# Kernel tuning notes

Measured on AMD Instinct MI355X. Metric: run time of the kernel, lower is better.

Reference implementation:

```python
import jax, jax.numpy as jnp
import numpy as np

T, B, V, E, H = 128, 32, 32000, 512, 1024
PAD = 0

def setup_inputs() -> dict:
    key = jax.random.key(0)
    ks = jax.random.split(key, 10)
    indices = jax.random.randint(ks[0], (T, B), 0, V)
    emb = jax.random.normal(ks[1], (V, E), jnp.float32) * 0.02
    s = 1.0 / np.sqrt(H).astype(np.float32)
    W_ih = jax.random.normal(ks[2], (4 * H, E), jnp.float32) * s
    W_hh = jax.random.normal(ks[3], (4 * H, H), jnp.float32) * s
    b_ih = jax.random.normal(ks[4], (4 * H,), jnp.float32) * 0.01
    b_hh = jax.random.normal(ks[5], (4 * H,), jnp.float32) * 0.01
    W_out = jax.random.normal(ks[6], (V, H), jnp.float32) * s
    b_out = jnp.zeros((V,), jnp.float32)
    h0 = jax.random.uniform(ks[7], (B, H), jnp.float32, -0.1, 0.1)
    c0 = jax.random.uniform(ks[8], (B, H), jnp.float32, -0.1, 0.1)
    return dict(indices=indices, emb=emb, W_ih=W_ih, W_hh=W_hh,
                b_ih=b_ih, b_hh=b_hh, W_out=W_out, b_out=b_out, h0=h0, c0=c0)

def reference(indices, emb, W_ih, W_hh, b_ih, b_hh, W_out, b_out, h0, c0):
    # embed + relu for all timesteps at once (dropout_rate=0.0 -> identity)
    x_all = jax.nn.relu(emb[indices[:-1]])   # [T-1, B, E]
    targets = indices[1:]                    # [T-1, B]

    def step(carry, inp):
        h, c, loss = carry
        x, tgt = inp
        # torch LSTM gate order: i, f, g, o
        gates = x @ W_ih.T + b_ih + h @ W_hh.T + b_hh   # [B, 4H]
        i, f, g, o = jnp.split(gates, 4, axis=-1)
        c = jax.nn.sigmoid(f) * c + jax.nn.sigmoid(i) * jnp.tanh(g)
        h = jax.nn.sigmoid(o) * jnp.tanh(c)
        logp = jax.nn.log_softmax(h @ W_out.T + b_out, axis=-1)  # [B, V]
        nll = -jnp.take_along_axis(logp, tgt[:, None], axis=-1)[:, 0]
        # NLLLoss(reduction='sum', ignore_index=PAD)
        loss = loss + jnp.sum(jnp.where(tgt != PAD, nll, 0.0))
        return (h, c, loss), None

    (_, _, loss), _ = jax.lax.scan(step, (h0, c0, jnp.float32(0.0)), (x_all, targets))
    return loss
```

## Files before the change

kernel.cpp:

```cpp
#include <hip/hip_runtime.h>
#include <hip/hip_bf16.h>
#include <hip/hip_cooperative_groups.h>
#include <math.h>

namespace cg = cooperative_groups;

typedef __bf16 bf16_t;
typedef bf16_t bf16x8 __attribute__((ext_vector_type(8)));
typedef float f32x4 __attribute__((ext_vector_type(4)));
typedef unsigned u32x2 __attribute__((ext_vector_type(2)));
typedef unsigned u32x4 __attribute__((ext_vector_type(4)));

#define T_SEQ 128
#define NB 32
#define NV 32000
#define NE 512
#define NH 1024
#define G4 4096
#define MROWS 4064
#define MPAD 4096

#define NBLK 256
#define SENT 0xFFFFFFFFu

__device__ __forceinline__ void g2lds16(const bf16_t* g, bf16_t* l) {
  __builtin_amdgcn_global_load_lds((const __attribute__((address_space(1))) void*)g,
                                   (__attribute__((address_space(3))) void*)l, 16, 0, 0);
}

__device__ __forceinline__ unsigned short bf16bits(float x) {
  bf16_t b = (bf16_t)x;
  return __builtin_bit_cast(unsigned short, b);
}

__device__ __forceinline__ void cvt4(const float* __restrict__ s,
                                     bf16_t* __restrict__ d, long j) {
  float4 v = *(const float4*)(s + j * 4);
  uint2 o;
  o.x = (unsigned)bf16bits(v.x) | ((unsigned)bf16bits(v.y) << 16);
  o.y = (unsigned)bf16bits(v.z) | ((unsigned)bf16bits(v.w) << 16);
  *(uint2*)(d + j * 4) = o;
}

__global__ void k_prep(const int* __restrict__ idx, const float* __restrict__ emb,
                       const float* __restrict__ W_ih, const float* __restrict__ W_hh,
                       const float* __restrict__ b_ih, const float* __restrict__ b_hh,
                       const float* __restrict__ W_out, const float* __restrict__ h0,
                       bf16_t* __restrict__ W_ih_bf, bf16_t* __restrict__ W_hh_bf,
                       bf16_t* __restrict__ W_out_bf, bf16_t* __restrict__ x_bf,
                       bf16_t* __restrict__ h_all, bf16_t* __restrict__ h0_bf,
                       float* __restrict__ bc, float* __restrict__ rowS,
                       int* __restrict__ tgt, unsigned* __restrict__ bar) {
  const long n4_Wih = 4096L * 512 / 4;
  const long n4_Whh = 4096L * 1024 / 4;
  const long n4_Wout = 32000L * 1024 / 4;
  const long n4_X = 4096L * 512 / 4;
  const long n4_H0 = 32L * 1024 / 4;
  const long n4_Hall = 4096L * 1024 / 8;
  const long nSentinel = 4064L * 128;
  const long nScal = 3 * 4096L + 1024;
  const long NTOT = n4_Wih + n4_Whh + n4_Wout + n4_X + n4_H0 + n4_Hall + nScal;
  long stride = (long)gridDim.x * blockDim.x;
  for (long i = (long)blockIdx.x * blockDim.x + threadIdx.x; i < NTOT; i += stride) {
    long j = i;
    if (j < n4_Wih) { cvt4(W_ih, W_ih_bf, j); continue; }
    j -= n4_Wih;
    if (j < n4_Whh) { cvt4(W_hh, W_hh_bf, j); continue; }
    j -= n4_Whh;
    if (j < n4_Wout) { cvt4(W_out, W_out_bf, j); continue; }
    j -= n4_Wout;
    if (j < n4_X) {
      long m = j >> 7; int e4 = (int)(j & 127);
      uint2 o; o.x = 0u; o.y = 0u;
      if (m < MROWS) {
        float4 v = *(const float4*)(emb + (long)idx[m] * NE + e4 * 4);
        v.x = fmaxf(v.x, 0.f); v.y = fmaxf(v.y, 0.f);
        v.z = fmaxf(v.z, 0.f); v.w = fmaxf(v.w, 0.f);
        o.x = (unsigned)bf16bits(v.x) | ((unsigned)bf16bits(v.y) << 16);
        o.y = (unsigned)bf16bits(v.z) | ((unsigned)bf16bits(v.w) << 16);
      }
      *(uint2*)(x_bf + m * 512 + e4 * 4) = o;
      continue;
    }
    j -= n4_X;
    if (j < n4_H0) { cvt4(h0, h0_bf, j); continue; }
    j -= n4_H0;
    if (j < n4_Hall) {
      unsigned v = (j < nSentinel) ? SENT : 0u;
      uint4 s; s.x = v; s.y = v; s.z = v; s.w = v;
      ((uint4*)h_all)[j] = s;
      continue;
    }
    j -= n4_Hall;
    if (j < 4096) { bc[j] = b_ih[j] + b_hh[j]; continue; }
    j -= 4096;
    if (j < 4096) { rowS[j] = 0.f; continue; }
    j -= 4096;
    if (j < 4096) { tgt[j] = (j < MROWS) ? idx[j + NB] : 0; continue; }
    j -= 4096;
    { bar[j] = 0u; continue; }
  }
}

__global__ __launch_bounds__(256) void k_gemm1(const bf16_t* __restrict__ A,
                                               const bf16_t* __restrict__ B,
                                               const float* __restrict__ bc,
                                               bf16_t* __restrict__ C) {
  const int K = 512;
  int tid = threadIdx.x, wid = tid >> 6, lane = tid & 63;
  int wm = wid & 1, wn = wid >> 1;
  int quad = lane >> 4, l15 = lane & 15;
  int mBase = blockIdx.x * 64, nBase = blockIdx.y * 128;

  const bf16x8* pa0 = (const bf16x8*)(A + (long)(mBase + wm * 32 + l15) * K + quad * 8);
  const bf16x8* pa1 = (const bf16x8*)(A + (long)(mBase + wm * 32 + 16 + l15) * K + quad * 8);
  const bf16x8* pb[4];
#pragma unroll
  for (int j = 0; j < 4; ++j)
    pb[j] = (const bf16x8*)(B + (long)(nBase + wn * 64 + j * 16 + l15) * K + quad * 8);

  f32x4 acc[2][4];
#pragma unroll
  for (int mi = 0; mi < 2; ++mi)
#pragma unroll
    for (int ni = 0; ni < 4; ++ni) acc[mi][ni] = (f32x4){0.f, 0.f, 0.f, 0.f};

  for (int kk = 0; kk < K / 32; ++kk) {
    bf16x8 a0 = pa0[kk * 4], a1 = pa1[kk * 4];
    bf16x8 b0 = pb[0][kk * 4], b1 = pb[1][kk * 4], b2 = pb[2][kk * 4], b3 = pb[3][kk * 4];
    acc[0][0] = __builtin_amdgcn_mfma_f32_16x16x32_bf16(a0, b0, acc[0][0], 0, 0, 0);
    acc[0][1] = __builtin_amdgcn_mfma_f32_16x16x32_bf16(a0, b1, acc[0][1], 0, 0, 0);
    acc[0][2] = __builtin_amdgcn_mfma_f32_16x16x32_bf16(a0, b2, acc[0][2], 0, 0, 0);
    acc[0][3] = __builtin_amdgcn_mfma_f32_16x16x32_bf16(a0, b3, acc[0][3], 0, 0, 0);
    acc[1][0] = __builtin_amdgcn_mfma_f32_16x16x32_bf16(a1, b0, acc[1][0], 0, 0, 0);
    acc[1][1] = __builtin_amdgcn_mfma_f32_16x16x32_bf16(a1, b1, acc[1][1], 0, 0, 0);
    acc[1][2] = __builtin_amdgcn_mfma_f32_16x16x32_bf16(a1, b2, acc[1][2], 0, 0, 0);
    acc[1][3] = __builtin_amdgcn_mfma_f32_16x16x32_bf16(a1, b3, acc[1][3], 0, 0, 0);
  }
#pragma unroll
  for (int ni = 0; ni < 4; ++ni) {
    int col = nBase + wn * 64 + ni * 16 + l15;
    float bcv = bc[col];
#pragma unroll
    for (int mi = 0; mi < 2; ++mi)
#pragma unroll
      for (int r = 0; r < 4; ++r) {
        int row = mBase + wm * 32 + mi * 16 + quad * 4 + r;
        C[(long)row * G4 + col] = (bf16_t)(acc[mi][ni][r] + bcv);
      }
  }
}

__global__ __launch_bounds__(512) void k_rec9(const bf16_t* __restrict__ gates_x,
                                              const bf16_t* __restrict__ W_hh_bf,
                                              const bf16_t* __restrict__ h0_bf,
                                              bf16_t* __restrict__ h_all,
                                              const float* __restrict__ c0,
                                              unsigned* __restrict__ bar) {
  __shared__ __align__(16) float red[32 * 68];

  int bid = blockIdx.x;
  int mi = bid & 1;
  int hb = bid >> 1;
  int gbase = hb * 8;
  int tid = threadIdx.x, wid = tid >> 6, lane = tid & 63;
  int cg = wid & 1, kh = wid >> 1;
  int quad = lane >> 4, l15 = lane & 15;

  unsigned* genp = bar + mi * 512 + 288;
  unsigned* flagp = bar + mi * 512 + 320 + hb;
  const unsigned* fp2 = bar + mi * 512 + 320 + (lane << 1);
  bool isagg = (bid < 2) && (wid == 7);

  int wrow = (cg ? 2048 : 0) + ((l15 & 8) ? 1024 : 0) + gbase + (l15 & 7);
  const bf16x8* pw = (const bf16x8*)(W_hh_bf + (long)wrow * NH + kh * 256 + quad * 8);
  bf16x8 wfrag[8];
#pragma unroll
  for (int kk = 0; kk < 8; ++kk) wfrag[kk] = pw[kk * 4];

  int pb = tid >> 2, pu2 = (tid & 3) * 2;
  int u0 = gbase + pu2;
  int bglob = mi * 16 + pb;
  float cst0 = 0.f, cst1 = 0.f;
  if (tid < 64) {
    cst0 = c0[(long)bglob * NH + u0];
    cst1 = c0[(long)bglob * NH + u0 + 1];
  }
  unsigned* h32 = (unsigned*)h_all;

  for (int t = 0; t < T_SEQ - 1; ++t) {
    unsigned gxi2 = 0, gxf2 = 0, gxg2 = 0, gxo2 = 0;
    if (tid < 64) {
      const unsigned* gp = (const unsigned*)(gates_x + (long)(t * NB + bglob) * G4);
      int q = u0 >> 1;
      gxi2 = gp[q]; gxf2 = gp[512 + q]; gxg2 = gp[1024 + q]; gxo2 = gp[1536 + q];
    }

    if (t > 0) {
      if (isagg) {
        unsigned need = (unsigned)t;
        while (1) {
          u32x2 fv;
          asm volatile("global_load_dwordx2 %0, %1, off sc0 sc1\n\t"
                       "s_waitcnt vmcnt(0)"
                       : "=&v"(fv) : "v"(fp2) : "memory");
          if (__all((fv.x >= need) & (fv.y >= need))) break;
          __builtin_amdgcn_s_sleep(1);
        }
        if (lane == 0)
          __hip_atomic_store(genp, (unsigned)t, __ATOMIC_RELAXED,
                             __HIP_MEMORY_SCOPE_AGENT);
      }
      if (tid == 0) {
        unsigned need = (unsigned)t;
        while (__hip_atomic_load(genp, __ATOMIC_RELAXED,
                                 __HIP_MEMORY_SCOPE_AGENT) < need)
          __builtin_amdgcn_s_sleep(1);
      }
    }
    __syncthreads();
    asm volatile("" ::: "memory");

    bf16x8 hfr[8];
    if (t == 0) {
      const bf16x8* pa0 =
          (const bf16x8*)(h0_bf + (long)(mi * 16 + l15) * NH + kh * 256 + quad * 8);
#pragma unroll
      for (int kk = 0; kk < 8; ++kk) hfr[kk] = pa0[kk * 4];
    } else {
      const bf16_t* hb8 = h_all + (long)(t - 1) * NB * NH +
                          (long)(mi * 16 + l15) * NH + kh * 256 + quad * 8;
      const bf16x8* pa = (const bf16x8*)hb8;
#pragma unroll
      for (int kk = 0; kk < 8; ++kk) hfr[kk] = pa[kk * 4];
      unsigned bad = 0;
#pragma unroll
      for (int kk = 0; kk < 8; ++kk) {
        u32x4 w = __builtin_bit_cast(u32x4, hfr[kk]);
        bad |= (unsigned)(w.x == SENT) | (unsigned)(w.y == SENT) |
               (unsigned)(w.z == SENT) | (unsigned)(w.w == SENT);
      }
      while (!__all(bad == 0)) {
        __builtin_amdgcn_s_sleep(1);
        u32x4 hw[8];
#pragma unroll
        for (int kk = 0; kk < 8; ++kk)
          asm volatile("global_load_dwordx4 %0, %1, off sc0 sc1"
                       : "=&v"(hw[kk]) : "v"(hb8 + kk * 32) : "memory");
        asm volatile("s_waitcnt vmcnt(0)" ::: "memory");
        bad = 0;
#pragma unroll
        for (int kk = 0; kk < 8; ++kk) {
          bad |= (unsigned)(hw[kk].x == SENT) | (unsigned)(hw[kk].y == SENT) |
                 (unsigned)(hw[kk].z == SENT) | (unsigned)(hw[kk].w == SENT);
          hfr[kk] = __builtin_bit_cast(bf16x8, hw[kk]);
        }
      }
    }

    f32x4 acc = (f32x4){0.f, 0.f, 0.f, 0.f};
#pragma unroll
    for (int kk = 0; kk < 8; ++kk)
      acc = __builtin_amdgcn_mfma_f32_16x16x32_bf16(hfr[kk], wfrag[kk], acc, 0, 0, 0);
#pragma unroll
    for (int r = 0; r < 4; ++r) {
      int row = (cg << 4) + (quad << 2) + r;
      red[row * 68 + (l15 << 2) + kh] = acc[r];
    }
    __syncthreads();

    if (tid < 64) {
      const float* rc = red;
      float hv[2];
#pragma unroll
      for (int d = 0; d < 2; ++d) {
        int q = pu2 + d;
        float4 vi = *(const float4*)(rc + pb * 68 + (q << 2));
        float4 vf = *(const float4*)(rc + pb * 68 + ((8 + q) << 2));
        float4 vg = *(const float4*)(rc + (16 + pb) * 68 + (q << 2));
        float4 vo = *(const float4*)(rc + (16 + pb) * 68 + ((8 + q) << 2));
        unsigned bi = d ? (gxi2 & 0xffff0000u) : (gxi2 << 16);
        unsigned bff = d ? (gxf2 & 0xffff0000u) : (gxf2 << 16);
        unsigned bg = d ? (gxg2 & 0xffff0000u) : (gxg2 << 16);
        unsigned bo = d ? (gxo2 & 0xffff0000u) : (gxo2 << 16);
        float iv = vi.x + vi.y + vi.z + vi.w + __builtin_bit_cast(float, bi);
        float fv = vf.x + vf.y + vf.z + vf.w + __builtin_bit_cast(float, bff);
        float gv = vg.x + vg.y + vg.z + vg.w + __builtin_bit_cast(float, bg);
        float ov = vo.x + vo.y + vo.z + vo.w + __builtin_bit_cast(float, bo);
        float si = 1.f / (1.f + __expf(-iv));
        float sf = 1.f / (1.f + __expf(-fv));
        float so = 1.f / (1.f + __expf(-ov));
        float tg = 1.f - 2.f / (__expf(2.f * gv) + 1.f);
        float& cs = d ? cst1 : cst0;
        cs = sf * cs + si * tg;
        float th = 1.f - 2.f / (__expf(2.f * cs) + 1.f);
        hv[d] = so * th;
      }
      unsigned pack = (unsigned)bf16bits(hv[0]) | ((unsigned)bf16bits(hv[1]) << 16);
      __hip_atomic_store(&h32[(long)(t * NB + bglob) * 512 + (u0 >> 1)], pack,
                         __ATOMIC_RELAXED, __HIP_MEMORY_SCOPE_AGENT);
      if (t < T_SEQ - 2 && tid == 0)
        __hip_atomic_store(flagp, (unsigned)(t + 1), __ATOMIC_RELAXED,
                           __HIP_MEMORY_SCOPE_AGENT);
    }
  }
}

__global__ __launch_bounds__(256) void k_gemm2(const bf16_t* __restrict__ A,
                                               const bf16_t* __restrict__ B,
                                               const float* __restrict__ b_out,
                                               float* __restrict__ rowS) {
  __shared__ bf16_t As[128 * 32];
  __shared__ bf16_t Bs[128 * 32];
  const int K = 1024;
  int tid = threadIdx.x, wid = tid >> 6, lane = tid & 63;
  int wm = wid & 1, wn = wid >> 1;
  int quad = lane >> 4, l15 = lane & 15;
  int mBase = blockIdx.x * 128, nBase = blockIdx.y * 128;

  int rc = lane >> 2, seg = lane & 3;
  int cA0 = 2 * wid, cA1 = 2 * wid + 1;
  const bf16_t* gA0 = A + (size_t)(mBase + cA0 * 16 + rc) * K + seg * 8;
  const bf16_t* gA1 = A + (size_t)(mBase + cA1 * 16 + rc) * K + seg * 8;
  const bf16_t* gB0 = B + (size_t)(nBase + cA0 * 16 + rc) * K + seg * 8;
  const bf16_t* gB1 = B + (size_t)(nBase + cA1 * 16 + rc) * K + seg * 8;
  bf16_t* lA0 = As + cA0 * 512;
  bf16_t* lA1 = As + cA1 * 512;
  bf16_t* lB0 = Bs + cA0 * 512;
  bf16_t* lB1 = Bs + cA1 * 512;

  const bf16x8* pa[4];
  const bf16x8* pbf[4];
#pragma unroll
  for (int i = 0; i < 4; ++i) {
    pa[i] = (const bf16x8*)(As + (wm * 64 + i * 16 + l15) * 32 + quad * 8);
    pbf[i] = (const bf16x8*)(Bs + (wn * 64 + i * 16 + l15) * 32 + quad * 8);
  }

  f32x4 acc[4][4];
#pragma unroll
  for (int i = 0; i < 4; ++i)
#pragma unroll
    for (int j = 0; j < 4; ++j) acc[i][j] = (f32x4){0.f, 0.f, 0.f, 0.f};

  for (int kt = 0; kt < K / 32; ++kt) {
    g2lds16(gA0 + kt * 32, lA0);
    g2lds16(gA1 + kt * 32, lA1);
    g2lds16(gB0 + kt * 32, lB0);
    g2lds16(gB1 + kt * 32, lB1);
    __syncthreads();

    bf16x8 af[4], bf[4];
#pragma unroll
    for (int i = 0; i < 4; ++i) { af[i] = *pa[i]; bf[i] = *pbf[i]; }
#pragma unroll
    for (int i = 0; i < 4; ++i)
#pragma unroll
      for (int j = 0; j < 4; ++j)
        acc[i][j] = __builtin_amdgcn_mfma_f32_16x16x32_bf16(af[i], bf[j], acc[i][j], 0, 0, 0);
    __syncthreads();
  }

#pragma unroll
  for (int i = 0; i < 4; ++i) {
    float rs[4] = {0.f, 0.f, 0.f, 0.f};
#pragma unroll
    for (int j = 0; j < 4; ++j) {
      int col = nBase + wn * 64 + j * 16 + l15;
      float bb = b_out[col];
#pragma unroll
      for (int r = 0; r < 4; ++r) rs[r] += __expf(acc[i][j][r] + bb);
    }
#pragma unroll
    for (int r = 0; r < 4; ++r) {
#pragma unroll
      for (int s = 1; s < 16; s <<= 1) rs[r] += __shfl_xor(rs[r], s);
      if (l15 == 0) {
        int row = mBase + wm * 64 + i * 16 + quad * 4 + r;
        if (row < MROWS) atomicAdd(&rowS[row], rs[r]);
      }
    }
  }
}

__global__ __launch_bounds__(256) void k_tgt(const bf16_t* __restrict__ h_all,
                                             const bf16_t* __restrict__ W_out_bf,
                                             const float* __restrict__ b_out,
                                             const int* __restrict__ tgt,
                                             float* __restrict__ tgt_logit) {
  int gw = (int)((blockIdx.x * blockDim.x + threadIdx.x) >> 6);
  int lane = threadIdx.x & 63;
  if (gw >= MROWS) return;
  int v = tgt[gw];
  const bf16x8* ph = (const bf16x8*)(h_all + (long)gw * NH + lane * 16);
  const bf16x8* pw = (const bf16x8*)(W_out_bf + (long)v * NH + lane * 16);
  float acc = 0.f;
#pragma unroll
  for (int j = 0; j < 2; ++j) {
    bf16x8 h8 = ph[j], w8 = pw[j];
#pragma unroll
    for (int q = 0; q < 8; ++q) acc += (float)h8[q] * (float)w8[q];
  }
#pragma unroll
  for (int s = 1; s < 64; s <<= 1) acc += __shfl_xor(acc, s);
  if (lane == 0) tgt_logit[gw] = acc + b_out[v];
}

__global__ __launch_bounds__(256) void k_loss(const float* __restrict__ rowS,
                                              const float* __restrict__ tl,
                                              const int* __restrict__ tgt,
                                              float* __restrict__ out) {
  __shared__ float sm[256];
  float s = 0.f;
  for (int i = threadIdx.x; i < MROWS; i += 256)
    if (tgt[i] != 0) s += logf(rowS[i]) - tl[i];
  sm[threadIdx.x] = s;
  __syncthreads();
  for (int off = 128; off > 0; off >>= 1) {
    if (threadIdx.x < off) sm[threadIdx.x] += sm[threadIdx.x + off];
    __syncthreads();
  }
  if (threadIdx.x == 0) out[0] = sm[0];
}

extern "C" void kernel_launch(void* const* d_in, const int* in_sizes, int n_in,
                              void* d_out, int out_size, void* d_ws, size_t ws_size,
                              hipStream_t stream) {
  const int* idx = (const int*)d_in[0];
  const float* emb = (const float*)d_in[1];
  const float* W_ih = (const float*)d_in[2];
  const float* W_hh = (const float*)d_in[3];
  const float* b_ih = (const float*)d_in[4];
  const float* b_hh = (const float*)d_in[5];
  const float* W_out = (const float*)d_in[6];
  const float* b_out = (const float*)d_in[7];
  const float* h0 = (const float*)d_in[8];
  const float* c0 = (const float*)d_in[9];

  char* ws = (char*)d_ws;
  bf16_t* W_ih_bf = (bf16_t*)ws;            ws += 4096L * 512 * 2;
  bf16_t* W_hh_bf = (bf16_t*)ws;            ws += 4096L * 1024 * 2;
  bf16_t* W_out_bf = (bf16_t*)ws;           ws += 32000L * 1024 * 2;
  bf16_t* x_bf = (bf16_t*)ws;               ws += 4096L * 512 * 2;
  bf16_t* gates_x = (bf16_t*)ws;            ws += 4096L * 4096 * 2;
  bf16_t* h_all = (bf16_t*)ws;              ws += 4096L * 1024 * 2;
  bf16_t* h0_bf = (bf16_t*)ws;              ws += 32L * 1024 * 2;
  float* bc = (float*)ws;                   ws += 4096L * 4;
  float* rowS = (float*)ws;                 ws += 4096L * 4;
  float* tgt_logit = (float*)ws;            ws += 4096L * 4;
  int* tgt = (int*)ws;                      ws += 4096L * 4;
  unsigned* bar = (unsigned*)ws;            ws += 1024L * 4;

  k_prep<<<4096, 256, 0, stream>>>(idx, emb, W_ih, W_hh, b_ih, b_hh, W_out, h0,
                                   W_ih_bf, W_hh_bf, W_out_bf, x_bf, h_all, h0_bf,
                                   bc, rowS, tgt, bar);

  k_gemm1<<<dim3(64, 32), 256, 0, stream>>>(x_bf, W_ih_bf, bc, gates_x);

  {
    void* args[] = {(void*)&gates_x, (void*)&W_hh_bf, (void*)&h0_bf, (void*)&h_all,
                    (void*)&c0, (void*)&bar};
    hipLaunchCooperativeKernel((void*)k_rec9, dim3(NBLK), dim3(512), args, 0, stream);
  }

  k_gemm2<<<dim3(32, 250), 256, 0, stream>>>(h_all, W_out_bf, b_out, rowS);

  k_tgt<<<1016, 256, 0, stream>>>(h_all, W_out_bf, b_out, tgt, tgt_logit);

  k_loss<<<1, 256, 0, stream>>>(rowS, tgt_logit, tgt, (float*)d_out);
}
```

Before: 1.261 ms.

## Retile output-projection GEMM to 256x256 with double-buffered swizzled LDS pipeline

The logits GEMM moves from 128x128 tiles with a K-step of 32 and single buffering to 256x256 tiles with a K-step of 64, using 512 threads and two LDS buffers. Loads for step kt+2 are issued while MFMAs run on the current buffer, with explicit waitcnt, barrier and priority control. An XOR swizzle on LDS columns is meant to avoid bank conflicts. The goal is more reuse of each loaded tile and hiding global-load latency, at the cost of 128KB of LDS per block and heavy register use, which may limit occupancy and leaves fewer blocks (2000) to spread across the GPU.

```diff
diff --git a/kernel.cpp b/kernel.cpp
--- a/kernel.cpp
+++ b/kernel.cpp
@@ -306,77 +306,119 @@
   }
 }
 
-__global__ __launch_bounds__(256) void k_gemm2(const bf16_t* __restrict__ A,
-                                               const bf16_t* __restrict__ B,
-                                               const float* __restrict__ b_out,
-                                               float* __restrict__ rowS) {
-  __shared__ bf16_t As[128 * 32];
-  __shared__ bf16_t Bs[128 * 32];
+__global__ __launch_bounds__(512, 2) void k_gemm2(const bf16_t* __restrict__ A,
+                                                  const bf16_t* __restrict__ B,
+                                                  const float* __restrict__ b_out,
+                                                  float* __restrict__ rowS) {
+  __shared__ bf16_t SA[2][256 * 64];
+  __shared__ bf16_t SB[2][256 * 64];
   const int K = 1024;
+  const int NT = 16;
   int tid = threadIdx.x, wid = tid >> 6, lane = tid & 63;
-  int wm = wid & 1, wn = wid >> 1;
+  int wm = wid >> 2, wn = wid & 3;
   int quad = lane >> 4, l15 = lane & 15;
-  int mBase = blockIdx.x * 128, nBase = blockIdx.y * 128;
-
-  int rc = lane >> 2, seg = lane & 3;
-  int cA0 = 2 * wid, cA1 = 2 * wid + 1;
-  const bf16_t* gA0 = A + (size_t)(mBase + cA0 * 16 + rc) * K + seg * 8;
-  const bf16_t* gA1 = A + (size_t)(mBase + cA1 * 16 + rc) * K + seg * 8;
-  const bf16_t* gB0 = B + (size_t)(nBase + cA0 * 16 + rc) * K + seg * 8;
-  const bf16_t* gB1 = B + (size_t)(nBase + cA1 * 16 + rc) * K + seg * 8;
-  bf16_t* lA0 = As + cA0 * 512;
-  bf16_t* lA1 = As + cA1 * 512;
-  bf16_t* lB0 = Bs + cA0 * 512;
-  bf16_t* lB1 = Bs + cA1 * 512;
-
-  const bf16x8* pa[4];
-  const bf16x8* pbf[4];
-#pragma unroll
-  for (int i = 0; i < 4; ++i) {
-    pa[i] = (const bf16x8*)(As + (wm * 64 + i * 16 + l15) * 32 + quad * 8);
-    pbf[i] = (const bf16x8*)(Bs + (wn * 64 + i * 16 + l15) * 32 + quad * 8);
-  }
-
-  f32x4 acc[4][4];
-#pragma unroll
-  for (int i = 0; i < 4; ++i)
+  int mBase = blockIdx.x * 256, nBase = blockIdx.y * 256;
+
+#define STAGE2(buf, kt)                                                       \
+  {                                                                           \
+    _Pragma("unroll") for (int r = 0; r < 4; ++r) {                           \
+      int o16 = r * 512 + tid;                                                \
+      int row = o16 >> 3;                                                     \
+      int col = ((o16 & 7) << 3) ^ (((row >> 2) & 1) << 4);                   \
+      g2lds16(A + (size_t)(mBase + row) * K + (kt) * 64 + col,                \
+              &SA[buf][(r * 512 + wid * 64) * 8]);                            \
+    }                                                                         \
+    _Pragma("unroll") for (int r = 0; r < 4; ++r) {                           \
+      int o16 = r * 512 + tid;                                                \
+      int row = o16 >> 3;                                                     \
+      int col = ((o16 & 7) << 3) ^ (((row >> 2) & 1) << 4);                   \
+      g2lds16(B + (size_t)(nBase + row) * K + (kt) * 64 + col,                \
+              &SB[buf][(r * 512 + wid * 64) * 8]);                            \
+    }                                                                         \
+  }
+
+  f32x4 acc[8][4];
+#pragma unroll
+  for (int i = 0; i < 8; ++i)
 #pragma unroll
     for (int j = 0; j < 4; ++j) acc[i][j] = (f32x4){0.f, 0.f, 0.f, 0.f};
 
-  for (int kt = 0; kt < K / 32; ++kt) {
-    g2lds16(gA0 + kt * 32, lA0);
-    g2lds16(gA1 + kt * 32, lA1);
-    g2lds16(gB0 + kt * 32, lB0);
-    g2lds16(gB1 + kt * 32, lB1);
-    __syncthreads();
-
-    bf16x8 af[4], bf[4];
-#pragma unroll
-    for (int i = 0; i < 4; ++i) { af[i] = *pa[i]; bf[i] = *pbf[i]; }
-#pragma unroll
-    for (int i = 0; i < 4; ++i)
-#pragma unroll
-      for (int j = 0; j < 4; ++j)
-        acc[i][j] = __builtin_amdgcn_mfma_f32_16x16x32_bf16(af[i], bf[j], acc[i][j], 0, 0, 0);
-    __syncthreads();
-  }
-
-#pragma unroll
-  for (int i = 0; i < 4; ++i) {
+  STAGE2(0, 0);
+  STAGE2(1, 1);
+  asm volatile("s_waitcnt vmcnt(8)" ::: "memory");
+  __builtin_amdgcn_s_barrier();
+
+  for (int kt = 0; kt < NT; ++kt) {
+    int cur = kt & 1;
+    const bf16_t* sa = SA[cur];
+    const bf16_t* sb = SB[cur];
+    bf16x8 af[8], bfr[4];
+#pragma unroll
+    for (int mf = 0; mf < 8; ++mf) {
+      int ra = wm * 128 + mf * 16 + l15;
+      int c = (quad * 8) ^ (((ra >> 2) & 1) << 4);
+      af[mf] = *(const bf16x8*)(sa + ra * 64 + c);
+    }
+#pragma unroll
+    for (int nf = 0; nf < 4; ++nf) {
+      int rb = wn * 64 + nf * 16 + l15;
+      int c = (quad * 8) ^ (((rb >> 2) & 1) << 4);
+      bfr[nf] = *(const bf16x8*)(sb + rb * 64 + c);
+    }
+#pragma unroll
+    for (int mf = 0; mf < 8; ++mf)
+#pragma unroll
+      for (int nf = 0; nf < 4; ++nf)
+        acc[mf][nf] =
+            __builtin_amdgcn_mfma_f32_16x16x32_bf16(af[mf], bfr[nf], acc[mf][nf], 0, 0, 0);
+#pragma unroll
+    for (int mf = 0; mf < 8; ++mf) {
+      int ra = wm * 128 + mf * 16 + l15;
+      int c = (32 + quad * 8) ^ (((ra >> 2) & 1) << 4);
+      af[mf] = *(const bf16x8*)(sa + ra * 64 + c);
+    }
+#pragma unroll
+    for (int nf = 0; nf < 4; ++nf) {
+      int rb = wn * 64 + nf * 16 + l15;
+      int c = (32 + quad * 8) ^ (((rb >> 2) & 1) << 4);
+      bfr[nf] = *(const bf16x8*)(sb + rb * 64 + c);
+    }
+    asm volatile("s_waitcnt lgkmcnt(0)" ::: "memory");
+    __builtin_amdgcn_sched_barrier(0);
+    __builtin_amdgcn_s_barrier();
+    if (kt + 2 < NT) STAGE2(cur, kt + 2);
+    __builtin_amdgcn_s_setprio(1);
+#pragma unroll
+    for (int mf = 0; mf < 8; ++mf)
+#pragma unroll
+      for (int nf = 0; nf < 4; ++nf)
+        acc[mf][nf] =
+            __builtin_amdgcn_mfma_f32_16x16x32_bf16(af[mf], bfr[nf], acc[mf][nf], 0, 0, 0);
+    __builtin_amdgcn_s_setprio(0);
+    if (kt + 2 < NT) {
+      asm volatile("s_waitcnt vmcnt(8)" ::: "memory");
+    } else {
+      asm volatile("s_waitcnt vmcnt(0)" ::: "memory");
+    }
+    __builtin_amdgcn_s_barrier();
+  }
+#undef STAGE2
+
+#pragma unroll
+  for (int mf = 0; mf < 8; ++mf) {
     float rs[4] = {0.f, 0.f, 0.f, 0.f};
 #pragma unroll
-    for (int j = 0; j < 4; ++j) {
-      int col = nBase + wn * 64 + j * 16 + l15;
-      float bb = b_out[col];
-#pragma unroll
-      for (int r = 0; r < 4; ++r) rs[r] += __expf(acc[i][j][r] + bb);
+    for (int nf = 0; nf < 4; ++nf) {
+      float bb = b_out[nBase + wn * 64 + nf * 16 + l15];
+#pragma unroll
+      for (int r = 0; r < 4; ++r) rs[r] += __expf(acc[mf][nf][r] + bb);
     }
 #pragma unroll
     for (int r = 0; r < 4; ++r) {
 #pragma unroll
       for (int s = 1; s < 16; s <<= 1) rs[r] += __shfl_xor(rs[r], s);
       if (l15 == 0) {
-        int row = mBase + wm * 64 + i * 16 + quad * 4 + r;
+        int row = mBase + wm * 128 + mf * 16 + quad * 4 + r;
         if (row < MROWS) atomicAdd(&rowS[row], rs[r]);
       }
     }
@@ -463,7 +505,7 @@
     hipLaunchCooperativeKernel((void*)k_rec9, dim3(NBLK), dim3(512), args, 0, stream);
   }
 
-  k_gemm2<<<dim3(32, 250), 256, 0, stream>>>(h_all, W_out_bf, b_out, rowS);
+  k_gemm2<<<dim3(16, 125), 512, 0, stream>>>(h_all, W_out_bf, b_out, rowS);
 
   k_tgt<<<1016, 256, 0, stream>>>(h_all, W_out_bf, b_out, tgt, tgt_logit);
 
```

Measured after the change: 1.243 ms. Within noise of the previous version (-1.4%).
